# Kernel optimization log

Measured on AMD Instinct MI355X. Metric: run time of the kernel, lower is better.

The kernel has to match this reference:

```python
import jax, jax.numpy as jnp
import numpy as np

N, E = 100000, 1600000
IN, OUT = 64, 64
R, B = 16, 4
EPS = 1e-5


def setup_inputs() -> dict:
    key = jax.random.key(0)
    ks = jax.random.split(key, 8)
    s_in = 1.0 / np.sqrt(IN)
    return {
        "node_feat": jax.random.normal(ks[0], (N, IN), jnp.float32),
        "bases": jax.random.normal(ks[1], (B, IN, OUT), jnp.float32) * s_in,
        "comp": jax.random.normal(ks[2], (R, B), jnp.float32) * (1.0 / np.sqrt(B)),
        "loop_weight": jax.random.normal(ks[3], (IN, OUT), jnp.float32) * s_in,
        "bias": jnp.zeros((OUT,), jnp.float32),
        "gamma": jnp.ones((OUT,), jnp.float32),
        "beta": jnp.zeros((OUT,), jnp.float32),
        "src": jax.random.randint(ks[4], (E,), 0, N, jnp.int32),
        "dst": jax.random.randint(ks[5], (E,), 0, N, jnp.int32),
        "edge_types": jax.random.randint(ks[6], (E,), 0, R, jnp.int32),
    }


def reference(node_feat, bases, comp, loop_weight, bias, gamma, beta, src, dst, edge_types):
    n = node_feat.shape[0]
    # basis decomposition: W_r = sum_b comp[r,b] * V_b  -> [R, in, out]
    W = jnp.einsum('rb,bio->rio', comp, bases)
    # per-node, per-relation transform (avoids [E,in,out] per-edge weight gather)
    h_all = jnp.einsum('ni,rio->nro', node_feat, W)        # [N, R, out]
    m = h_all[src, edge_types]                             # [E, out] per-edge messages
    agg = jax.ops.segment_sum(m, dst, num_segments=n)      # scatter-add to dst
    out = agg + node_feat @ loop_weight + bias             # self-loop + bias (DGL defaults)
    out = jnp.where(out >= 0, out, 0.1 * out)              # LeakyReLU(0.1)
    mu = jnp.mean(out, axis=-1, keepdims=True)
    var = jnp.mean(jnp.square(out - mu), axis=-1, keepdims=True)
    return (out - mu) * jax.lax.rsqrt(var + EPS) * gamma + beta
```

## Files before the change

kernel.cpp:

```cpp
#include <hip/hip_runtime.h>

#define N_NODES 100000
#define N_EDGES 1600000
#define NBINS   100000
#define LN_EPS  1e-5f

#define NG 8
#define NS 32
#define RANGE 12500
#define SLICE_I4 12500
#define SCAN_BLOCKS 98

#define XB_BLOCKS   64

typedef unsigned int u32;
typedef unsigned short u16;
typedef __attribute__((ext_vector_type(8))) short short8;
typedef __attribute__((ext_vector_type(4))) float f32x4;

__device__ __forceinline__ u16 f2bf(float f) {
    u32 u = __float_as_uint(f);
    u32 r = (u + 0x7FFFu + ((u >> 16) & 1u)) >> 16;
    return (u16)r;
}
__device__ __forceinline__ float bf2f(u16 h) {
    return __uint_as_float((u32)h << 16);
}

__global__ __launch_bounds__(1024) void k_prep_hist(
    const float* __restrict__ x, const float* __restrict__ bases,
    const float* __restrict__ loopw, const int* __restrict__ dst,
    u16* __restrict__ wf, u16* __restrict__ xb, u32* __restrict__ priv)
{
    __shared__ u32 lh[RANGE];
    const int t = threadIdx.x;
    if (blockIdx.x < NG * NS) {
        for (int j = t; j < RANGE; j += 1024) lh[j] = 0u;
        __syncthreads();
        const int s = blockIdx.x & (NS - 1);
        const int g = blockIdx.x >> 5;
        const int lo = g * RANGE;
        const int4* dst4 = (const int4*)dst;
        const int i0 = s * SLICE_I4;
        for (int i = i0 + t; i < i0 + SLICE_I4; i += 1024) {
            const int4 d4 = dst4[i];
#pragma unroll
            for (int q = 0; q < 4; ++q) {
                const int d = (q == 0) ? d4.x : (q == 1) ? d4.y
                            : (q == 2) ? d4.z : d4.w;
                const u32 rel = (u32)(d - lo);
                if (rel < (u32)RANGE) atomicAdd(&lh[rel], 1u);
            }
        }
        __syncthreads();
        u32* pb = priv + (size_t)(g * NS + s) * RANGE;
        for (int j = t; j < RANGE; j += 1024) pb[j] = lh[j];
    } else if (blockIdx.x == NG * NS) {
        for (int idx = t; idx < 4 * 10 * 64 * 8; idx += 1024) {
            const int j = idx & 7;
            const int l = (idx >> 3) & 63;
            const int rest = idx >> 9;
            const int ks = rest % 10;
            const int ct = rest / 10;
            const int k = ks * 32 + (l >> 4) * 8 + j;
            const int c = ct * 16 + (l & 15);
            float v;
            if (k < 256) v = bases[(k & 3) * 4096 + (k >> 2) * 64 + c];
            else         v = loopw[(k - 256) * 64 + c];
            wf[idx] = f2bf(v);
        }
    } else {
        const int bb = blockIdx.x - NG * NS - 1;
        for (int i = bb * 1024 + t; i < N_NODES * 16; i += XB_BLOCKS * 1024) {
            const float4 v = ((const float4*)x)[i];
            uint2 w;
            w.x = (u32)f2bf(v.x) | ((u32)f2bf(v.y) << 16);
            w.y = (u32)f2bf(v.z) | ((u32)f2bf(v.w) << 16);
            ((uint2*)xb)[i] = w;
        }
    }
}

__global__ __launch_bounds__(1024) void k_scan_block(
    u32* __restrict__ priv, u32* __restrict__ counts,
    u32* __restrict__ offs, u32* __restrict__ bsums)
{
    __shared__ u32 wsum[16];
    const int t = threadIdx.x;
    const int lane = t & 63, wid = t >> 6;
    const int idx = blockIdx.x * 1024 + t;
    u32 sv[NS];
    u32 v = 0u;
    u32 g = 0, local = 0;
    if (idx < NBINS) {
        g = (u32)idx / (u32)RANGE;
        local = (u32)idx - g * (u32)RANGE;
#pragma unroll
        for (int s = 0; s < NS; ++s) {
            sv[s] = priv[(size_t)(g * NS + s) * RANGE + local];
            v += sv[s];
        }
    }
    u32 sc = v;
#pragma unroll
    for (int off = 1; off < 64; off <<= 1) {
        u32 u = __shfl_up(sc, off, 64);
        if (lane >= off) sc += u;
    }
    if (lane == 63) wsum[wid] = sc;
    __syncthreads();
    if (wid == 0) {
        u32 w = (lane < 16) ? wsum[lane] : 0u;
#pragma unroll
        for (int off = 1; off < 16; off <<= 1) {
            u32 u = __shfl_up(w, off, 64);
            if (lane >= off) w += u;
        }
        if (lane < 16) wsum[lane] = w;
    }
    __syncthreads();
    const u32 prefix = (wid > 0) ? wsum[wid - 1] : 0u;
    const u32 incl = sc + prefix;
    const u32 excl = incl - v;
    if (idx < NBINS) {
        offs[idx] = excl;
        counts[idx] = v;
        u32 run = excl;
#pragma unroll
        for (int s = 0; s < NS; ++s) {
            priv[(size_t)(g * NS + s) * RANGE + local] = run;
            run += sv[s];
        }
    }
    if (t == 1023) bsums[blockIdx.x] = incl;
}

__global__ __launch_bounds__(1024) void k_scatter(
    const int* __restrict__ dst, const int* __restrict__ src,
    const int* __restrict__ et,
    const u32* __restrict__ priv, const u32* __restrict__ bsums,
    u32* __restrict__ boffs, u32* __restrict__ packed)
{
    __shared__ u32 cur[RANGE];
    __shared__ u32 sb[128];
    const int t = threadIdx.x;
    if (t < 64) {
        const u32 a = (t < SCAN_BLOCKS) ? bsums[t] : 0u;
        u32 s1 = a;
#pragma unroll
        for (int off = 1; off < 64; off <<= 1) {
            u32 u = __shfl_up(s1, off, 64);
            if (t >= off) s1 += u;
        }
        sb[t] = s1 - a;
        const u32 tot0 = __shfl(s1, 63, 64);
        const int t2 = t + 64;
        const u32 b = (t2 < SCAN_BLOCKS) ? bsums[t2] : 0u;
        u32 s2 = b;
#pragma unroll
        for (int off = 1; off < 64; off <<= 1) {
            u32 u = __shfl_up(s2, off, 64);
            if (t >= off) s2 += u;
        }
        sb[t2] = tot0 + s2 - b;
    }
    __syncthreads();

    const int s = blockIdx.x & (NS - 1);
    const int g = blockIdx.x >> 5;
    const int lo = g * RANGE;
    if (blockIdx.x == 0) {
        if (t < 128) boffs[t] = sb[t];
    }
    const u32* pb = priv + (size_t)(g * NS + s) * RANGE;
    for (int j = t; j < RANGE; j += 1024)
        cur[j] = pb[j] + sb[(lo + j) >> 10];
    __syncthreads();
    const int4* dst4 = (const int4*)dst;
    const int4* src4 = (const int4*)src;
    const int4* et4  = (const int4*)et;
    const int i0 = s * SLICE_I4;
    for (int i = i0 + t; i < i0 + SLICE_I4; i += 1024) {
        const int4 d4 = dst4[i];
        const int4 s4 = src4[i];
        const int4 e4 = et4[i];
#pragma unroll
        for (int q = 0; q < 4; ++q) {
            const int d = (q == 0) ? d4.x : (q == 1) ? d4.y
                        : (q == 2) ? d4.z : d4.w;
            const int sn = (q == 0) ? s4.x : (q == 1) ? s4.y
                         : (q == 2) ? s4.z : s4.w;
            const int ev = (q == 0) ? e4.x : (q == 1) ? e4.y
                         : (q == 2) ? e4.z : e4.w;
            const u32 rel = (u32)(d - lo);
            if (rel < (u32)RANGE) {
                const u32 pos = atomicAdd(&cur[rel], 1u);
                packed[pos] = (u32)sn | ((u32)ev << 20);
            }
        }
    }
}

__global__ __launch_bounds__(256) void k_agg(
    const u16* __restrict__ xb, const float4* __restrict__ comp,
    const u32* __restrict__ packed,
    const u32* __restrict__ offs, const u32* __restrict__ boffs,
    const u32* __restrict__ counts,
    uint2* __restrict__ y)
{
    const int t = threadIdx.x;
    const int lane = t & 63;
    const int wid = t >> 6;
    const int waves = gridDim.x * 4;
    const u16* xbl = xb + lane;

    for (int n0 = blockIdx.x * 4 + wid; n0 < N_NODES; n0 += waves) {
        const int n = __builtin_amdgcn_readfirstlane(n0);
        const u32 deg = counts[n];
        const u32 base = offs[n] + boffs[n >> 10];
        float a0 = 0.f, a1 = 0.f, a2 = 0.f, a3 = 0.f;
        u32 done = 0;
        while (done < deg) {
            u32 cnt = deg - done;
            if (cnt > 64u) cnt = 64u;
            const u32 li = ((u32)lane < cnt) ? (u32)lane : 0u;
            const u32 recs = packed[base + done + li];
            u32 k = 0;
            for (; k + 8 <= cnt; k += 8) {
                u32 rr[8];
#pragma unroll
                for (int q = 0; q < 8; ++q)
                    rr[q] = (u32)__builtin_amdgcn_readlane((int)recs, (int)(k + q));
                u16 hv[8];
#pragma unroll
                for (int q = 0; q < 8; ++q)
                    hv[q] = xbl[(size_t)(rr[q] & 0xFFFFFu) * 64];
                float4 cc[8];
#pragma unroll
                for (int q = 0; q < 8; ++q) cc[q] = comp[rr[q] >> 20];
#pragma unroll
                for (int q = 0; q < 8; ++q) {
                    const float xf = bf2f(hv[q]);
                    a0 = fmaf(cc[q].x, xf, a0);
                    a1 = fmaf(cc[q].y, xf, a1);
                    a2 = fmaf(cc[q].z, xf, a2);
                    a3 = fmaf(cc[q].w, xf, a3);
                }
            }
            for (; k < cnt; ++k) {
                const u32 r0 = (u32)__builtin_amdgcn_readlane((int)recs, (int)k);
                const float4 c0 = comp[r0 >> 20];
                const float xf = bf2f(xbl[(size_t)(r0 & 0xFFFFFu) * 64]);
                a0 = fmaf(c0.x, xf, a0);
                a1 = fmaf(c0.y, xf, a1);
                a2 = fmaf(c0.z, xf, a2);
                a3 = fmaf(c0.w, xf, a3);
            }
            done += cnt;
        }
        uint2 w;
        w.x = (u32)f2bf(a0) | ((u32)f2bf(a1) << 16);
        w.y = (u32)f2bf(a2) | ((u32)f2bf(a3) << 16);
        y[(size_t)n * 64 + lane] = w;
    }
}

__global__ __launch_bounds__(256) void k_gemm_ln(
    const short8* __restrict__ yf,
    const short8* __restrict__ xbf,
    const short8* __restrict__ wf,
    const float* __restrict__ bias, const float* __restrict__ gamma,
    const float* __restrict__ beta, float* __restrict__ out)
{
    const int lane = threadIdx.x & 63;
    const int wid = threadIdx.x >> 6;
    const int m = lane & 15, kg = lane >> 4;
    float bsv[4], gm[4], bt[4];
#pragma unroll
    for (int ct = 0; ct < 4; ++ct) {
        bsv[ct] = bias[ct * 16 + m];
        gm[ct] = gamma[ct * 16 + m];
        bt[ct] = beta[ct * 16 + m];
    }
    const int ntiles = N_NODES / 16;
    for (int tile = blockIdx.x * 4 + wid; tile < ntiles; tile += gridDim.x * 4) {
        const int base = tile * 16;
        const int row = base + m;
        short8 a[10];
#pragma unroll
        for (int ks = 0; ks < 8; ++ks)
            a[ks] = yf[(size_t)row * 32 + ks * 4 + kg];
        a[8] = xbf[(size_t)row * 8 + kg];
        a[9] = xbf[(size_t)row * 8 + 4 + kg];
        f32x4 acc[4];
#pragma unroll
        for (int ct = 0; ct < 4; ++ct) {
            acc[ct] = (f32x4){0.f, 0.f, 0.f, 0.f};
#pragma unroll
            for (int ks = 0; ks < 10; ++ks)
                acc[ct] = __builtin_amdgcn_mfma_f32_16x16x32_bf16(
                    a[ks], wf[(ct * 10 + ks) * 64 + lane], acc[ct], 0, 0, 0);
        }
        float v[4][4];
#pragma unroll
        for (int ct = 0; ct < 4; ++ct)
#pragma unroll
            for (int r = 0; r < 4; ++r) {
                const float u = acc[ct][r] + bsv[ct];
                v[ct][r] = (u >= 0.f) ? u : 0.1f * u;
            }
#pragma unroll
        for (int r = 0; r < 4; ++r) {
            float s1 = v[0][r] + v[1][r] + v[2][r] + v[3][r];
#pragma unroll
            for (int mk = 1; mk < 16; mk <<= 1) s1 += __shfl_xor(s1, mk, 64);
            const float mu = s1 * (1.f / 64.f);
            float s2 = 0.f;
#pragma unroll
            for (int ct = 0; ct < 4; ++ct) {
                const float d = v[ct][r] - mu;
                s2 += d * d;
            }
#pragma unroll
            for (int mk = 1; mk < 16; mk <<= 1) s2 += __shfl_xor(s2, mk, 64);
            const float rstd = rsqrtf(s2 * (1.f / 64.f) + LN_EPS);
            const int ro = base + kg * 4 + r;
#pragma unroll
            for (int ct = 0; ct < 4; ++ct)
                out[(size_t)ro * 64 + ct * 16 + m] =
                    (v[ct][r] - mu) * rstd * gm[ct] + bt[ct];
        }
    }
}

__global__ __launch_bounds__(256) void k_edge_direct(
    const float* __restrict__ x, const float* __restrict__ bases,
    const float* __restrict__ comp,
    const int* __restrict__ src, const int* __restrict__ dst,
    const int* __restrict__ et, float* __restrict__ agg)
{
    const int lane = threadIdx.x & 63;
    int e = blockIdx.x * 4 + (threadIdx.x >> 6);
    if (e >= N_EDGES) return;
    e = __builtin_amdgcn_readfirstlane(e);
    const int s = src[e], d = dst[e], r = et[e];
    const float4 c = *(const float4*)(comp + r * 4);
    const float* xr = x + (size_t)s * 64;
    float acc = 0.f;
    for (int i = 0; i < 64; ++i) {
        const float w = c.x * bases[i * 64 + lane]
                      + c.y * bases[4096 + i * 64 + lane]
                      + c.z * bases[8192 + i * 64 + lane]
                      + c.w * bases[12288 + i * 64 + lane];
        acc = fmaf(xr[i], w, acc);
    }
    atomicAdd(&agg[(size_t)d * 64 + lane], acc);
}

__global__ __launch_bounds__(256) void k_finalize(
    const float* __restrict__ x, const float* __restrict__ loopw,
    const float* __restrict__ bias, const float* __restrict__ gamma,
    const float* __restrict__ beta, float* __restrict__ out)
{
    const int t = threadIdx.x;
    const int lane = t & 63;
    const int wid = t >> 6;
    float wreg[64];
#pragma unroll
    for (int i = 0; i < 64; ++i)
        wreg[i] = loopw[i * 64 + lane];
    const float bs = bias[lane], gm = gamma[lane], bt = beta[lane];
    const int waves = gridDim.x * 4;
    for (int n = blockIdx.x * 4 + wid; n < N_NODES; n += waves) {
        float xv = x[(size_t)n * 64 + lane];
        const int xbv = __float_as_int(xv);
        float slv = bs;
#pragma unroll
        for (int i = 0; i < 64; ++i) {
            const float s = __int_as_float(__builtin_amdgcn_readlane(xbv, i));
            slv = fmaf(s, wreg[i], slv);
        }
        float v = out[(size_t)n * 64 + lane] + slv;
        v = (v >= 0.f) ? v : 0.1f * v;
        float s1 = v;
#pragma unroll
        for (int mm = 32; mm >= 1; mm >>= 1) s1 += __shfl_xor(s1, mm, 64);
        const float mu = s1 * (1.f / 64.f);
        const float dv = v - mu;
        float s2 = dv * dv;
#pragma unroll
        for (int mm = 32; mm >= 1; mm >>= 1) s2 += __shfl_xor(s2, mm, 64);
        const float var = s2 * (1.f / 64.f);
        out[(size_t)n * 64 + lane] = dv * rsqrtf(var + LN_EPS) * gm + bt;
    }
}

extern "C" void kernel_launch(void* const* d_in, const int* in_sizes, int n_in,
                              void* d_out, int out_size, void* d_ws, size_t ws_size,
                              hipStream_t stream) {
    const float* x     = (const float*)d_in[0];
    const float* bases = (const float*)d_in[1];
    const float* comp  = (const float*)d_in[2];
    const float* loopw = (const float*)d_in[3];
    const float* bias  = (const float*)d_in[4];
    const float* gamma = (const float*)d_in[5];
    const float* beta  = (const float*)d_in[6];
    const int*   src   = (const int*)d_in[7];
    const int*   dst   = (const int*)d_in[8];
    const int*   et    = (const int*)d_in[9];
    float* out = (float*)d_out;

    size_t p = 0;
    auto alloc = [&](size_t bytes) {
        size_t cur = p;
        p = (p + bytes + 255) & ~(size_t)255;
        return cur;
    };
    char* ws = (char*)d_ws;
    const size_t o_counts = alloc((size_t)NBINS * sizeof(u32));
    const size_t o_wf     = alloc((size_t)4 * 10 * 64 * 8 * sizeof(u16));
    const size_t o_xb     = alloc((size_t)N_NODES * 64 * sizeof(u16));
    const size_t o_y      = alloc((size_t)N_NODES * 256 * sizeof(u16));
    const size_t o_priv   = alloc((size_t)NG * NS * RANGE * sizeof(u32));
    const size_t o_offs   = alloc((size_t)NBINS * sizeof(u32));
    const size_t o_bsums  = alloc(128 * sizeof(u32));
    const size_t o_boffs  = alloc(128 * sizeof(u32));
    const size_t o_packed = alloc((size_t)N_EDGES * sizeof(u32));
    const size_t need = p;

    if (ws_size >= need) {
        u32* counts = (u32*)(ws + o_counts);
        u16* wfp    = (u16*)(ws + o_wf);
        u16* xb     = (u16*)(ws + o_xb);
        u16* y      = (u16*)(ws + o_y);
        u32* priv   = (u32*)(ws + o_priv);
        u32* offs   = (u32*)(ws + o_offs);
        u32* bsums  = (u32*)(ws + o_bsums);
        u32* boffs  = (u32*)(ws + o_boffs);
        u32* packed = (u32*)(ws + o_packed);

        k_prep_hist<<<NG * NS + 1 + XB_BLOCKS, 1024, 0, stream>>>(
            x, bases, loopw, dst, wfp, xb, priv);
        k_scan_block<<<SCAN_BLOCKS, 1024, 0, stream>>>(priv, counts, offs, bsums);
        k_scatter<<<NG * NS, 1024, 0, stream>>>(dst, src, et, priv, bsums,
                                                boffs, packed);
        k_agg<<<2048, 256, 0, stream>>>(xb, (const float4*)comp, packed,
                                        offs, boffs, counts, (uint2*)y);
        k_gemm_ln<<<(N_NODES / 16 + 3) / 4, 256, 0, stream>>>(
            (const short8*)y, (const short8*)xb, (const short8*)wfp,
            bias, gamma, beta, out);
    } else {
        hipMemsetAsync(d_out, 0, (size_t)N_NODES * 64 * sizeof(float), stream);
        k_edge_direct<<<(N_EDGES + 3) / 4, 256, 0, stream>>>(
            x, bases, comp, src, dst, et, out);
        k_finalize<<<2048, 256, 0, stream>>>(x, loopw, bias, gamma, beta, out);
    }
}
```

Baseline: 130.1 us.

## Assign contiguous node ranges per wave and stream edges across node boundaries

Each wave now handles a fixed contiguous run of 13 nodes instead of grid-striding one node at a time. It walks the combined CSR edge range in 64-record chunks, so records from neighbouring nodes share a single coalesced load and low-degree nodes don't waste most of a 64-lane fetch. The next chunk of records is prefetched while the current one is processed. In exchange, control flow gets more complex with per-node boundary tracking, and the fixed node-per-wave partition can unbalance load.

```diff
diff --git a/kernel.cpp b/kernel.cpp
--- a/kernel.cpp
+++ b/kernel.cpp
@@ -12,6 +12,8 @@
 #define SCAN_BLOCKS 98
 
 #define XB_BLOCKS   64
+#define AGG_BLOCKS  2048
+#define NPW 13
 
 typedef unsigned int u32;
 typedef unsigned short u16;
@@ -211,22 +213,49 @@
     const int t = threadIdx.x;
     const int lane = t & 63;
     const int wid = t >> 6;
-    const int waves = gridDim.x * 4;
     const u16* xbl = xb + lane;
 
-    for (int n0 = blockIdx.x * 4 + wid; n0 < N_NODES; n0 += waves) {
-        const int n = __builtin_amdgcn_readfirstlane(n0);
-        const u32 deg = counts[n];
-        const u32 base = offs[n] + boffs[n >> 10];
-        float a0 = 0.f, a1 = 0.f, a2 = 0.f, a3 = 0.f;
-        u32 done = 0;
-        while (done < deg) {
-            u32 cnt = deg - done;
-            if (cnt > 64u) cnt = 64u;
-            const u32 li = ((u32)lane < cnt) ? (u32)lane : 0u;
-            const u32 recs = packed[base + done + li];
-            u32 k = 0;
-            for (; k + 8 <= cnt; k += 8) {
+    int w = blockIdx.x * 4 + wid;
+    w = __builtin_amdgcn_readfirstlane(w);
+    int n = w * NPW;
+    if (n >= N_NODES) return;
+    const int nEnd = (n + NPW < N_NODES) ? n + NPW : N_NODES;
+
+    const u32 base = offs[n] + boffs[n >> 10];
+    const u32 end  = (nEnd < N_NODES) ? offs[nEnd] + boffs[nEnd >> 10]
+                                      : (u32)N_EDGES;
+    const u32 total = end - base;
+
+    float a0 = 0.f, a1 = 0.f, a2 = 0.f, a3 = 0.f;
+    u32 r = 0;
+    while (n < nEnd) {
+        r = counts[n];
+        if (r) break;
+        y[(size_t)n * 64 + lane] = (uint2){0u, 0u};
+        ++n;
+    }
+
+    u32 idx0 = base + (u32)lane;
+    if (idx0 > (u32)(N_EDGES - 1)) idx0 = (u32)(N_EDGES - 1);
+    u32 recs = packed[idx0];
+
+    u32 done = 0;
+    while (done < total) {
+        u32 cnt = total - done;
+        if (cnt > 64u) cnt = 64u;
+        const u32 nd = done + cnt;
+        u32 recs_next = 0u;
+        if (nd < total) {
+            u32 idx = base + nd + (u32)lane;
+            if (idx > (u32)(N_EDGES - 1)) idx = (u32)(N_EDGES - 1);
+            recs_next = packed[idx];
+        }
+        u32 k = 0;
+        while (k < cnt) {
+            if (r == 0u) break;
+            u32 m = (r < cnt - k) ? r : (cnt - k);
+            const u32 kend = k + m;
+            for (; k + 8 <= kend; k += 8) {
                 u32 rr[8];
 #pragma unroll
                 for (int q = 0; q < 8; ++q)
@@ -247,7 +276,7 @@
                     a3 = fmaf(cc[q].w, xf, a3);
                 }
             }
-            for (; k < cnt; ++k) {
+            for (; k < kend; ++k) {
                 const u32 r0 = (u32)__builtin_amdgcn_readlane((int)recs, (int)k);
                 const float4 c0 = comp[r0 >> 20];
                 const float xf = bf2f(xbl[(size_t)(r0 & 0xFFFFFu) * 64]);
@@ -256,12 +285,24 @@
                 a2 = fmaf(c0.z, xf, a2);
                 a3 = fmaf(c0.w, xf, a3);
             }
-            done += cnt;
-        }
-        uint2 w;
-        w.x = (u32)f2bf(a0) | ((u32)f2bf(a1) << 16);
-        w.y = (u32)f2bf(a2) | ((u32)f2bf(a3) << 16);
-        y[(size_t)n * 64 + lane] = w;
+            r -= m;
+            if (r == 0u) {
+                uint2 wv;
+                wv.x = (u32)f2bf(a0) | ((u32)f2bf(a1) << 16);
+                wv.y = (u32)f2bf(a2) | ((u32)f2bf(a3) << 16);
+                y[(size_t)n * 64 + lane] = wv;
+                a0 = a1 = a2 = a3 = 0.f;
+                ++n;
+                while (n < nEnd) {
+                    r = counts[n];
+                    if (r) break;
+                    y[(size_t)n * 64 + lane] = (uint2){0u, 0u};
+                    ++n;
+                }
+            }
+        }
+        done = nd;
+        recs = recs_next;
     }
 }
 
@@ -444,8 +485,8 @@
         k_scan_block<<<SCAN_BLOCKS, 1024, 0, stream>>>(priv, counts, offs, bsums);
         k_scatter<<<NG * NS, 1024, 0, stream>>>(dst, src, et, priv, bsums,
                                                 boffs, packed);
-        k_agg<<<2048, 256, 0, stream>>>(xb, (const float4*)comp, packed,
-                                        offs, boffs, counts, (uint2*)y);
+        k_agg<<<AGG_BLOCKS, 256, 0, stream>>>(xb, (const float4*)comp, packed,
+                                              offs, boffs, counts, (uint2*)y);
         k_gemm_ln<<<(N_NODES / 16 + 3) / 4, 256, 0, stream>>>(
             (const short8*)y, (const short8*)xb, (const short8*)wfp,
             bias, gamma, beta, out);
```

New measurement: 130.2 us. No clear change (+0.0%).
